# Kernel optimization log

Measured on AMD Instinct MI355X. Metric: run time of the kernel, lower is better.

Reference implementation:

```python
import jax, jax.numpy as jnp
import numpy as np
import math

B, D, TX, TY = 16, 192, 512, 2048
NEG = -1e9


def _neg_cent(x_mean, x_logs, z):
    # x_mean, x_logs: [B, D, TX]; z: [B, D, TY] -> neg_cent: [B, TY, TX]
    s_p_sq_r = jnp.exp(-2.0 * x_logs)                                   # [B,D,TX]
    nc1 = jnp.sum(-0.5 * math.log(2.0 * math.pi) - x_logs, axis=1, keepdims=True)  # [B,1,TX]
    nc2 = jnp.einsum('bdy,bdx->byx', -0.5 * z * z, s_p_sq_r)            # [B,TY,TX]
    nc3 = jnp.einsum('bdy,bdx->byx', z, x_mean * s_p_sq_r)              # [B,TY,TX]
    nc4 = jnp.sum(-0.5 * x_mean * x_mean * s_p_sq_r, axis=1, keepdims=True)  # [B,1,TX]
    return nc1 + nc2 + nc3 + nc4


def _mas_single(nc):
    # Monotonic alignment search (Viterbi DP) for one sample. nc: [TY, TX]
    ty, tx = nc.shape
    xs = jnp.arange(tx)

    def fwd_step(v_prev, inp):
        nc_row, y = inp
        v_diag = jnp.concatenate([jnp.full((1,), NEG, nc.dtype), v_prev[:-1]])
        take_diag = v_diag > v_prev                                      # bool [TX]
        v = nc_row + jnp.maximum(v_prev, v_diag)
        v = jnp.where(xs <= y, v, NEG)                                   # path cannot be ahead of time
        return v, take_diag

    v0 = jnp.where(xs == 0, nc[0], NEG)
    _, dirs = jax.lax.scan(fwd_step, v0, (nc[1:], jnp.arange(1, ty)))    # dirs: [TY-1, TX]

    def bwd_step(idx, d_row):
        # idx = path position at row y; move to y-1
        new_idx = idx - d_row[idx].astype(idx.dtype)
        return new_idx, idx

    idx0, path_tail = jax.lax.scan(bwd_step, jnp.array(tx - 1, jnp.int32), dirs, reverse=True)
    path = jnp.concatenate([idx0[None], path_tail])                      # [TY]
    return jax.nn.one_hot(path, tx, dtype=nc.dtype)                      # [TY, TX]


def _forward(x_mean, x_logs, z, logw):
    neg_cent = jax.lax.stop_gradient(_neg_cent(x_mean, x_logs, z))
    attn = jax.lax.stop_gradient(jax.vmap(_mas_single)(neg_cent))        # [B,TY,TX]
    w = jnp.sum(attn, axis=1, keepdims=True)                             # [B,1,TX] durations
    logw_ = jnp.log(w + 1e-6)
    l_length = jnp.sum((logw - logw_) ** 2, axis=(1, 2))                 # [B]
    m_p = jnp.einsum('byx,bdx->bdy', attn, x_mean)                       # [B,D,TY]
    logs_p = jnp.einsum('byx,bdx->bdy', attn, x_logs)                    # [B,D,TY]
    out_main = jnp.concatenate([m_p, logs_p], axis=1)                    # [B,2D,TY]
    return out_main, l_length, attn


def setup_inputs() -> dict:
    key = jax.random.key(0)
    k1, k2, k3, k4 = jax.random.split(key, 4)
    return {
        'x_mean': jax.random.normal(k1, (B, D, TX), jnp.float32),
        'x_logs': jax.random.normal(k2, (B, D, TX), jnp.float32),
        'z': jax.random.normal(k3, (B, D, TY), jnp.float32),
        'logw': jax.random.normal(k4, (B, 1, TX), jnp.float32),
    }


def reference(x_mean, x_logs, z, logw):
    return _forward(x_mean, x_logs, z, logw)
```

## Files before the change

### kernel.cpp

```cpp
#include <hip/hip_runtime.h>
#include <hip/hip_bf16.h>
#include <math.h>

#define B_   16
#define D_   192
#define TX_  512
#define TY_  2048
#define NEGV (-1e9f)



typedef __attribute__((address_space(1))) const float glob_f;
typedef __attribute__((address_space(3))) float       lds_f;

__global__ __launch_bounds__(512) void precomp(const float* __restrict__ xm,
                                               const float* __restrict__ xl,
                                               float* __restrict__ S,
                                               float* __restrict__ MS,
                                               float* __restrict__ Cpart) {
    int b = blockIdx.x;
    int p = blockIdx.y;
    int x = threadIdx.x;
    size_t base = ((size_t)b * D_ + p * 32) * TX_;
    const float* mb = xm + base;
    const float* lb = xl + base;
    float* Sb  = S  + base;
    float* MSb = MS + base;
    float c = 0.f;
    for (int d = 0; d < 32; d++) {
        float lg = lb[d * TX_ + x];
        float mn = mb[d * TX_ + x];
        float s  = expf(-2.f * lg);
        float ms = mn * s;
        Sb[d * TX_ + x]  = s;
        MSb[d * TX_ + x] = ms;
        c += -0.9189385332046727f - lg - 0.5f * mn * mn * s;
    }
    Cpart[(b * 6 + p) * TX_ + x] = c;
}

__global__ __launch_bounds__(256) void gemm_nc(const float* __restrict__ z,
                                               const float* __restrict__ S,
                                               const float* __restrict__ MS,
                                               const float* __restrict__ Cpart,
                                               float* __restrict__ NC) {
    int bx = blockIdx.x;
    int by = blockIdx.y;
    int b  = blockIdx.z;
    int tid = threadIdx.x;
    int tx = tid & 15, ty = tid >> 4;
    __shared__ __align__(16) float Zt[16 * 128];
    __shared__ __align__(16) float St[16 * 128];
    __shared__ __align__(16) float MSt[16 * 128];

    float acc[8][8];
#pragma unroll
    for (int i = 0; i < 8; i++)
#pragma unroll
        for (int j = 0; j < 8; j++) acc[i][j] = 0.f;

    int x0 = bx * 128, y0 = by * 128;
    const float* zb  = z  + (size_t)b * D_ * TY_;
    const float* Sb  = S  + (size_t)b * D_ * TX_;
    const float* MSb = MS + (size_t)b * D_ * TX_;

    for (int k0 = 0; k0 < D_; k0 += 16) {
#pragma unroll
        for (int j = 0; j < 2; j++) {
            int f = tid + j * 256;
            int kk = f >> 5, c = (f & 31) * 4;
            __builtin_amdgcn_global_load_lds((glob_f*)(zb  + (size_t)(k0 + kk) * TY_ + y0 + c),
                                             (lds_f*)(Zt  + f * 4), 16, 0, 0);
            __builtin_amdgcn_global_load_lds((glob_f*)(Sb  + (size_t)(k0 + kk) * TX_ + x0 + c),
                                             (lds_f*)(St  + f * 4), 16, 0, 0);
            __builtin_amdgcn_global_load_lds((glob_f*)(MSb + (size_t)(k0 + kk) * TX_ + x0 + c),
                                             (lds_f*)(MSt + f * 4), 16, 0, 0);
        }
        __syncthreads();

#pragma unroll 2
        for (int kk = 0; kk < 16; kk++) {
            float4 z0 = *(const float4*)&Zt[kk * 128 + ty * 4];
            float4 z1 = *(const float4*)&Zt[kk * 128 + 64 + ty * 4];
            float4 s0 = *(const float4*)&St[kk * 128 + tx * 4];
            float4 s1 = *(const float4*)&St[kk * 128 + 64 + tx * 4];
            float4 m0 = *(const float4*)&MSt[kk * 128 + tx * 4];
            float4 m1 = *(const float4*)&MSt[kk * 128 + 64 + tx * 4];
            float4 u0, u1;
            u0.x = -0.5f * z0.x * z0.x; u0.y = -0.5f * z0.y * z0.y;
            u0.z = -0.5f * z0.z * z0.z; u0.w = -0.5f * z0.w * z0.w;
            u1.x = -0.5f * z1.x * z1.x; u1.y = -0.5f * z1.y * z1.y;
            u1.z = -0.5f * z1.z * z1.z; u1.w = -0.5f * z1.w * z1.w;
            float zz[8] = {z0.x, z0.y, z0.z, z0.w, z1.x, z1.y, z1.z, z1.w};
            float uu[8] = {u0.x, u0.y, u0.z, u0.w, u1.x, u1.y, u1.z, u1.w};
            float ss[8] = {s0.x, s0.y, s0.z, s0.w, s1.x, s1.y, s1.z, s1.w};
            float mm[8] = {m0.x, m0.y, m0.z, m0.w, m1.x, m1.y, m1.z, m1.w};
#pragma unroll
            for (int i = 0; i < 8; i++)
#pragma unroll
                for (int j = 0; j < 8; j++)
                    acc[i][j] += uu[i] * ss[j] + zz[i] * mm[j];
        }
        __syncthreads();
    }

    float cv[8] = {0, 0, 0, 0, 0, 0, 0, 0};
#pragma unroll
    for (int p = 0; p < 6; p++) {
        float4 c0 = *(const float4*)&Cpart[(b * 6 + p) * TX_ + x0 + tx * 4];
        float4 c1 = *(const float4*)&Cpart[(b * 6 + p) * TX_ + x0 + 64 + tx * 4];
        cv[0] += c0.x; cv[1] += c0.y; cv[2] += c0.z; cv[3] += c0.w;
        cv[4] += c1.x; cv[5] += c1.y; cv[6] += c1.z; cv[7] += c1.w;
    }

#pragma unroll
    for (int i = 0; i < 8; i++) {
        int y = y0 + ty * 4 + (i & 3) + 64 * (i >> 2);
        float4 o0, o1;
        o0.x = acc[i][0] + cv[0]; o0.y = acc[i][1] + cv[1];
        o0.z = acc[i][2] + cv[2]; o0.w = acc[i][3] + cv[3];
        o1.x = acc[i][4] + cv[4]; o1.y = acc[i][5] + cv[5];
        o1.z = acc[i][6] + cv[6]; o1.w = acc[i][7] + cv[7];
        *(float4*)&NC[((size_t)b * TY_ + y) * TX_ + x0 + tx * 4]      = o0;
        *(float4*)&NC[((size_t)b * TY_ + y) * TX_ + x0 + 64 + tx * 4] = o1;
    }
}

__global__ __launch_bounds__(64, 1) void mas_forward(const float* __restrict__ NC,
                                                     unsigned char* __restrict__ dirs) {
    int b = blockIdx.x;
    int lane = threadIdx.x;
    const float* ncb = NC + (size_t)b * TY_ * TX_;
    const float4* base = (const float4*)ncb + lane * 2;

    float4 A[16], C[16];
#pragma unroll
    for (int s = 0; s < 16; s++) {
        A[s] = base[(size_t)(1 + s) * 128];
        C[s] = base[(size_t)(1 + s) * 128 + 1];
    }

    float v[8];
#pragma unroll
    for (int j = 0; j < 8; j++) v[j] = NEGV;
    if (lane == 0) v[0] = ncb[0];

    unsigned char* db = dirs + (size_t)b * 2048 * 64 + lane;

    float bound = NEGV;

    auto row_step = [&](float4 a, float4 c, int y, bool mask) {
        float ncv[8] = {a.x, a.y, a.z, a.w, c.x, c.y, c.z, c.w};
        float vd0 = (lane == 0) ? NEGV : bound;
        float v6o = v[6], v7o = v[7];
        float v7n = ncv[7] + fmaxf(v7o, v6o);
        if (mask && y < 511 && lane * 8 + 7 > y) v7n = NEGV;
        bound = __shfl_up(v7n, 1);
        unsigned bits = (v6o > v7o) ? 0x80u : 0u;
        float vd = vd0;
#pragma unroll
        for (int j = 0; j < 7; j++) {
            float vp = v[j];
            bits |= (vd > vp) ? (1u << j) : 0u;
            v[j] = ncv[j] + fmaxf(vp, vd);
            vd = vp;
        }
        if (mask && y < 511) {
            int xb = lane * 8;
#pragma unroll
            for (int j = 0; j < 7; j++)
                if (xb + j > y) v[j] = NEGV;
        }
        v[7] = v7n;
        db[(size_t)(y - 1) * 64] = (unsigned char)bits;
    };

    int y = 1;
    for (int k = 0; k < 32; k++) {
#pragma unroll
        for (int s = 0; s < 16; s++) {
            float4 a = A[s], c = C[s];
            A[s] = base[(size_t)(y + 16) * 128];
            C[s] = base[(size_t)(y + 16) * 128 + 1];
            row_step(a, c, y, true);
            y++;
        }
    }
    for (int k = 32; k < 127; k++) {
#pragma unroll
        for (int s = 0; s < 16; s++) {
            float4 a = A[s], c = C[s];
            A[s] = base[(size_t)(y + 16) * 128];
            C[s] = base[(size_t)(y + 16) * 128 + 1];
            row_step(a, c, y, false);
            y++;
        }
    }
#pragma unroll
    for (int s = 0; s < 15; s++) {
        row_step(A[s], C[s], y, false);
        y++;
    }
}

__global__ __launch_bounds__(64, 1) void mas_backtrack(const unsigned* __restrict__ dirs,
                                                       int* __restrict__ path) {
    int b = blockIdx.x;
    int lane = threadIdx.x;
    const unsigned* db = dirs + (size_t)b * 2048 * 16;
    int idx = TX_ - 1;

    for (int y_hi = 2047; y_hi >= 1; y_hi -= 64) {
        int wb = (idx >> 5) - 2;
        if (wb < 0) wb = 0;
        int base = wb << 5;
        int y = y_hi - lane;
        unsigned w0 = 0, w1 = 0, w2 = 0;
        if (y >= 1) {
            const unsigned* r = db + (size_t)(y - 1) * 16 + wb;
            w0 = r[0]; w1 = r[1]; w2 = r[2];
        }
        int steps = (y_hi < 64) ? y_hi : 64;
        int my_path = 0;
#pragma unroll 8
        for (int t = 0; t < steps; t++) {
            if (lane == t) my_path = idx;
            unsigned u0 = (unsigned)__shfl((int)w0, t);
            unsigned u1 = (unsigned)__shfl((int)w1, t);
            unsigned u2 = (unsigned)__shfl((int)w2, t);
            int off = idx - base;
            unsigned w = (off < 32) ? u0 : ((off < 64) ? u1 : u2);
            idx -= (int)((w >> (off & 31)) & 1u);
        }
        if (lane < steps) path[b * TY_ + (y_hi - lane)] = my_path;
    }
    if (lane == 0) path[b * TY_ + 0] = idx;
}

__global__ __launch_bounds__(512) void durations_ll(const int* __restrict__ path,
                                                    const float* __restrict__ logw,
                                                    float* __restrict__ out_l) {
    int b = blockIdx.x;
    int tid = threadIdx.x;
    __shared__ int wcnt[TX_];
    __shared__ float partial[8];
    wcnt[tid] = 0;
    __syncthreads();
    for (int y = tid; y < TY_; y += 512)
        atomicAdd(&wcnt[path[b * TY_ + y]], 1);
    __syncthreads();
    float t = logw[b * TX_ + tid] - logf((float)wcnt[tid] + 1e-6f);
    float sq = t * t;
#pragma unroll
    for (int off = 32; off > 0; off >>= 1) sq += __shfl_down(sq, off);
    if ((tid & 63) == 0) partial[tid >> 6] = sq;
    __syncthreads();
    if (tid == 0) {
        float s = 0.f;
#pragma unroll
        for (int i = 0; i < 8; i++) s += partial[i];
        out_l[b] = s;
    }
}

__global__ __launch_bounds__(256) void gather_main(const int* __restrict__ path,
                                                   const float* __restrict__ xm,
                                                   const float* __restrict__ xl,
                                                   float* __restrict__ out) {
    int c = blockIdx.x;
    int b = blockIdx.y;
    int tid = threadIdx.x;
    const float* src = (c < D_) ? (xm + ((size_t)b * D_ + c) * TX_)
                                : (xl + ((size_t)b * D_ + (c - D_)) * TX_);
    const int* pb = path + b * TY_;
    float* ob = out + ((size_t)b * 2 * D_ + c) * TY_;
#pragma unroll
    for (int k = 0; k < 8; k++) {
        int y = tid + k * 256;
        ob[y] = src[pb[y]];
    }
}

__global__ __launch_bounds__(128) void write_attn(const int* __restrict__ path,
                                                  float* __restrict__ attn) {
    int blk = blockIdx.x;
    int b = blk >> 11;
    int y = blk & 2047;
    int tid = threadIdx.x;
    int p = path[b * TY_ + y];
    float4 val = make_float4(0.f, 0.f, 0.f, 0.f);
    if ((p >> 2) == tid) {
        int r = p & 3;
        if (r == 0) val.x = 1.f;
        else if (r == 1) val.y = 1.f;
        else if (r == 2) val.z = 1.f;
        else val.w = 1.f;
    }
    ((float4*)attn)[((size_t)blk) * 128 + tid] = val;
}

extern "C" void kernel_launch(void* const* d_in, const int* in_sizes, int n_in,
                              void* d_out, int out_size, void* d_ws, size_t ws_size,
                              hipStream_t stream) {
    const float* x_mean = (const float*)d_in[0];
    const float* x_logs = (const float*)d_in[1];
    const float* z      = (const float*)d_in[2];
    const float* logw   = (const float*)d_in[3];
    float* out = (float*)d_out;

    char* ws = (char*)d_ws;
    float* S            = (float*)(ws + 0);
    float* MS           = (float*)(ws + 6291456);
    float* NC           = (float*)(ws + 12615680);
    unsigned char* dirs = (unsigned char*)(ws + 79724544);
    float* Cpart        = (float*)(ws + 79724544);
    int* path           = (int*)(ws + 81821696);

    float* out_main = out;
    float* out_l    = out + 12582912;
    float* out_attn = out + 12582928;

    precomp<<<dim3(B_, 6), dim3(512), 0, stream>>>(x_mean, x_logs, S, MS, Cpart);
    gemm_nc<<<dim3(4, 16, 16), dim3(256), 0, stream>>>(z, S, MS, Cpart, NC);
    mas_forward<<<dim3(B_), dim3(64), 0, stream>>>(NC, dirs);
    mas_backtrack<<<dim3(B_), dim3(64), 0, stream>>>((const unsigned*)dirs, path);
    durations_ll<<<dim3(B_), dim3(512), 0, stream>>>(path, logw, out_l);
    gather_main<<<dim3(384, 16), dim3(256), 0, stream>>>(path, x_mean, x_logs, out_main);
    write_attn<<<dim3(B_ * TY_), dim3(128), 0, stream>>>(path, out_attn);
}
```

Baseline: 763.1 us.

## Stage MAS forward rows through an LDS ring via async global-to-LDS loads

Replaces the 16-row register prefetch in the Viterbi forward kernel with a 16-slot LDS ring buffer. Rows are filled 12 rows ahead using global_load_lds, and waits are controlled with explicit s_waitcnt vmcnt counts. Rows are read back from LDS into a three-deep register rotation. The aim is to keep global-memory latency off the serial row chain while cutting register pressure. The cost is an LDS read on every row, and correctness now depends on the hand-tuned vmcnt thresholds, which also count the per-row direction stores.

```diff
diff --git a/kernel.cpp b/kernel.cpp
--- a/kernel.cpp
+++ b/kernel.cpp
@@ -126,19 +126,15 @@
     }
 }
 
+#define RING 16
+#define PF   12
+
 __global__ __launch_bounds__(64, 1) void mas_forward(const float* __restrict__ NC,
                                                      unsigned char* __restrict__ dirs) {
     int b = blockIdx.x;
     int lane = threadIdx.x;
     const float* ncb = NC + (size_t)b * TY_ * TX_;
-    const float4* base = (const float4*)ncb + lane * 2;
-
-    float4 A[16], C[16];
-#pragma unroll
-    for (int s = 0; s < 16; s++) {
-        A[s] = base[(size_t)(1 + s) * 128];
-        C[s] = base[(size_t)(1 + s) * 128 + 1];
-    }
+    __shared__ __align__(16) float ring[RING * TX_];
 
     float v[8];
 #pragma unroll
@@ -146,8 +142,22 @@
     if (lane == 0) v[0] = ncb[0];
 
     unsigned char* db = dirs + (size_t)b * 2048 * 64 + lane;
-
     float bound = NEGV;
+
+    auto stage = [&](int row) {
+        int slot = row & (RING - 1);
+        const float* src = ncb + (size_t)row * TX_ + lane * 4;
+        __builtin_amdgcn_global_load_lds((glob_f*)src,
+                                         (lds_f*)&ring[slot * TX_], 16, 0, 0);
+        __builtin_amdgcn_global_load_lds((glob_f*)(src + 256),
+                                         (lds_f*)&ring[slot * TX_ + 256], 16, 0, 0);
+    };
+
+    auto lds_row = [&](int row, float4& a, float4& c) {
+        int slot = row & (RING - 1);
+        a = *(const float4*)&ring[slot * TX_ + lane * 8];
+        c = *(const float4*)&ring[slot * TX_ + lane * 8 + 4];
+    };
 
     auto row_step = [&](float4 a, float4 c, int y, bool mask) {
         float ncv[8] = {a.x, a.y, a.z, a.w, c.x, c.y, c.z, c.w};
@@ -175,32 +185,48 @@
         db[(size_t)(y - 1) * 64] = (unsigned char)bits;
     };
 
+#pragma unroll
+    for (int r = 1; r <= PF; r++) stage(r);
+    asm volatile("s_waitcnt vmcnt(0)" ::: "memory");
+
+    float4 a0, c0, a1, c1, a2, c2;
+    lds_row(1, a0, c0);
+    lds_row(2, a1, c1);
+
     int y = 1;
-    for (int k = 0; k < 32; k++) {
-#pragma unroll
-        for (int s = 0; s < 16; s++) {
-            float4 a = A[s], c = C[s];
-            A[s] = base[(size_t)(y + 16) * 128];
-            C[s] = base[(size_t)(y + 16) * 128 + 1];
-            row_step(a, c, y, true);
-            y++;
-        }
-    }
-    for (int k = 32; k < 127; k++) {
-#pragma unroll
-        for (int s = 0; s < 16; s++) {
-            float4 a = A[s], c = C[s];
-            A[s] = base[(size_t)(y + 16) * 128];
-            C[s] = base[(size_t)(y + 16) * 128 + 1];
-            row_step(a, c, y, false);
-            y++;
-        }
-    }
-#pragma unroll
-    for (int s = 0; s < 15; s++) {
-        row_step(A[s], C[s], y, false);
-        y++;
-    }
+    for (int t = 0; t < 170; t++) {
+        asm volatile("s_waitcnt vmcnt(28)" ::: "memory");
+        lds_row(y + 2, a2, c2);
+        stage(y + PF);
+        row_step(a0, c0, y, true); y++;
+
+        asm volatile("s_waitcnt vmcnt(28)" ::: "memory");
+        lds_row(y + 2, a0, c0);
+        stage(y + PF);
+        row_step(a1, c1, y, true); y++;
+
+        asm volatile("s_waitcnt vmcnt(28)" ::: "memory");
+        lds_row(y + 2, a1, c1);
+        stage(y + PF);
+        row_step(a2, c2, y, true); y++;
+    }
+    for (int t = 0; t < 512; t++) {
+        asm volatile("s_waitcnt vmcnt(28)" ::: "memory");
+        lds_row(y + 2, a2, c2);
+        stage(min(y + PF, TY_ - 1));
+        row_step(a0, c0, y, false); y++;
+
+        asm volatile("s_waitcnt vmcnt(28)" ::: "memory");
+        lds_row(min(y + 2, TY_ - 1), a0, c0);
+        stage(min(y + PF, TY_ - 1));
+        row_step(a1, c1, y, false); y++;
+
+        asm volatile("s_waitcnt vmcnt(28)" ::: "memory");
+        lds_row(min(y + 2, TY_ - 1), a1, c1);
+        stage(min(y + PF, TY_ - 1));
+        row_step(a2, c2, y, false); y++;
+    }
+    row_step(a0, c0, 2047, false);
 }
 
 __global__ __launch_bounds__(64, 1) void mas_backtrack(const unsigned* __restrict__ dirs,
```

Measured after the change: 1.058 ms. 1.39x slower.

## Hand-pipeline MAS forward loads with inline asm and explicit vmcnt waits

Applied to the files above, without the earlier changes.

Rewrites the serial Viterbi forward kernel to issue global row loads and direction-byte stores through inline asm, keeping a 16-row register ring. Partial s_waitcnt vmcnt(45) waits replace the compiler's conservative full waits, so loads for later rows stay in flight while the current row is computed. It also adds index clamps in backtrack, durations and gather as safety guards. The hand-counted vmcnt is fragile: it relies on the exact count of outstanding loads and stores, and an error would read data before it arrives.

```diff
diff --git a/kernel.cpp b/kernel.cpp
--- a/kernel.cpp
+++ b/kernel.cpp
@@ -12,6 +12,7 @@
 
 typedef __attribute__((address_space(1))) const float glob_f;
 typedef __attribute__((address_space(3))) float       lds_f;
+typedef float f32x4 __attribute__((ext_vector_type(4)));
 
 __global__ __launch_bounds__(512) void precomp(const float* __restrict__ xm,
                                                const float* __restrict__ xl,
@@ -131,25 +132,19 @@
     int b = blockIdx.x;
     int lane = threadIdx.x;
     const float* ncb = NC + (size_t)b * TY_ * TX_;
-    const float4* base = (const float4*)ncb + lane * 2;
-
-    float4 A[16], C[16];
-#pragma unroll
-    for (int s = 0; s < 16; s++) {
-        A[s] = base[(size_t)(1 + s) * 128];
-        C[s] = base[(size_t)(1 + s) * 128 + 1];
-    }
+    int voff = lane * 32;
+
+    float nc00 = ncb[0];
+    asm volatile("" :: "v"(nc00));
 
     float v[8];
 #pragma unroll
     for (int j = 0; j < 8; j++) v[j] = NEGV;
-    if (lane == 0) v[0] = ncb[0];
-
-    unsigned char* db = dirs + (size_t)b * 2048 * 64 + lane;
+    if (lane == 0) v[0] = nc00;
 
     float bound = NEGV;
 
-    auto row_step = [&](float4 a, float4 c, int y, bool mask) {
+    auto row_step = [&](f32x4 a, f32x4 c, int y, bool mask) -> unsigned {
         float ncv[8] = {a.x, a.y, a.z, a.w, c.x, c.y, c.z, c.w};
         float vd0 = (lane == 0) ? NEGV : bound;
         float v6o = v[6], v7o = v[7];
@@ -172,35 +167,113 @@
                 if (xb + j > y) v[j] = NEGV;
         }
         v[7] = v7n;
-        db[(size_t)(y - 1) * 64] = (unsigned char)bits;
+        return bits;
     };
 
+    f32x4 r0a, r0c, r1a, r1c, r2a, r2c, r3a, r3c, r4a, r4c, r5a, r5c, r6a, r6c, r7a, r7c;
+    f32x4 r8a, r8c, r9a, r9c, r10a, r10c, r11a, r11c, r12a, r12c, r13a, r13c, r14a, r14c, r15a, r15c;
+
+    const float* pf = ncb + TX_;
+    unsigned char* dp = dirs + (size_t)b * 2048 * 64;
+
+#define LOADPAIR(RA, RC)                                                   \
+    do {                                                                   \
+        asm volatile("global_load_dwordx4 %0, %2, %1 offset:0"             \
+                     : "=v"(RA) : "s"(pf), "v"(voff));                     \
+        asm volatile("global_load_dwordx4 %0, %2, %1 offset:16"            \
+                     : "=v"(RC) : "s"(pf), "v"(voff));                     \
+        pf += TX_;                                                         \
+    } while (0)
+
+#define STOREBITS(BITS)                                                    \
+    asm volatile("global_store_byte %1, %2, %0" :: "s"(dp), "v"(lane), "v"(BITS))
+
+#define PHASE(RA, RC, MASKED)                                              \
+    do {                                                                   \
+        asm volatile("s_waitcnt vmcnt(45)" : "+v"(RA), "+v"(RC));          \
+        __builtin_amdgcn_sched_barrier(0);                                 \
+        unsigned bits_ = row_step(RA, RC, y, MASKED);                      \
+        STOREBITS(bits_);                                                  \
+        LOADPAIR(RA, RC);                                                  \
+        dp += 64;                                                          \
+        y++;                                                               \
+    } while (0)
+
+#define PH16(MASKED)                                                       \
+    PHASE(r0a, r0c, MASKED);  PHASE(r1a, r1c, MASKED);                     \
+    PHASE(r2a, r2c, MASKED);  PHASE(r3a, r3c, MASKED);                     \
+    PHASE(r4a, r4c, MASKED);  PHASE(r5a, r5c, MASKED);                     \
+    PHASE(r6a, r6c, MASKED);  PHASE(r7a, r7c, MASKED);                     \
+    PHASE(r8a, r8c, MASKED);  PHASE(r9a, r9c, MASKED);                     \
+    PHASE(r10a, r10c, MASKED); PHASE(r11a, r11c, MASKED);                  \
+    PHASE(r12a, r12c, MASKED); PHASE(r13a, r13c, MASKED);                  \
+    PHASE(r14a, r14c, MASKED); PHASE(r15a, r15c, MASKED);
+
+    LOADPAIR(r0a, r0c);   LOADPAIR(r1a, r1c);   LOADPAIR(r2a, r2c);   LOADPAIR(r3a, r3c);
+    LOADPAIR(r4a, r4c);   LOADPAIR(r5a, r5c);   LOADPAIR(r6a, r6c);   LOADPAIR(r7a, r7c);
+    LOADPAIR(r8a, r8c);   LOADPAIR(r9a, r9c);   LOADPAIR(r10a, r10c); LOADPAIR(r11a, r11c);
+    LOADPAIR(r12a, r12c); LOADPAIR(r13a, r13c); LOADPAIR(r14a, r14c); LOADPAIR(r15a, r15c);
+    asm volatile("s_waitcnt vmcnt(0)" ::: "memory");
+    __builtin_amdgcn_sched_barrier(0);
+
     int y = 1;
-    for (int k = 0; k < 32; k++) {
-#pragma unroll
-        for (int s = 0; s < 16; s++) {
-            float4 a = A[s], c = C[s];
-            A[s] = base[(size_t)(y + 16) * 128];
-            C[s] = base[(size_t)(y + 16) * 128 + 1];
-            row_step(a, c, y, true);
-            y++;
-        }
-    }
-    for (int k = 32; k < 127; k++) {
-#pragma unroll
-        for (int s = 0; s < 16; s++) {
-            float4 a = A[s], c = C[s];
-            A[s] = base[(size_t)(y + 16) * 128];
-            C[s] = base[(size_t)(y + 16) * 128 + 1];
-            row_step(a, c, y, false);
-            y++;
-        }
-    }
-#pragma unroll
-    for (int s = 0; s < 15; s++) {
-        row_step(A[s], C[s], y, false);
+    for (int t = 0; t < 32; t++) {
+        PH16(true)
+    }
+    for (int t = 32; t < 126; t++) {
+        PH16(false)
+    }
+    PHASE(r0a, r0c, false);  PHASE(r1a, r1c, false);
+    PHASE(r2a, r2c, false);  PHASE(r3a, r3c, false);
+    PHASE(r4a, r4c, false);  PHASE(r5a, r5c, false);
+    PHASE(r6a, r6c, false);  PHASE(r7a, r7c, false);
+    PHASE(r8a, r8c, false);  PHASE(r9a, r9c, false);
+    PHASE(r10a, r10c, false); PHASE(r11a, r11c, false);
+    PHASE(r12a, r12c, false); PHASE(r13a, r13c, false);
+    PHASE(r14a, r14c, false);
+    {
+        asm volatile("s_waitcnt vmcnt(45)" : "+v"(r15a), "+v"(r15c));
+        __builtin_amdgcn_sched_barrier(0);
+        unsigned bits_ = row_step(r15a, r15c, y, false);
+        STOREBITS(bits_);
+        dp += 64;
         y++;
     }
+
+    asm volatile("s_waitcnt vmcnt(1)"
+                 : "+v"(r0a), "+v"(r0c), "+v"(r1a), "+v"(r1c),
+                   "+v"(r2a), "+v"(r2c), "+v"(r3a), "+v"(r3c),
+                   "+v"(r4a), "+v"(r4c), "+v"(r5a), "+v"(r5c),
+                   "+v"(r6a), "+v"(r6c), "+v"(r7a), "+v"(r7c));
+    asm volatile("s_waitcnt vmcnt(1)"
+                 : "+v"(r8a), "+v"(r8c), "+v"(r9a), "+v"(r9c),
+                   "+v"(r10a), "+v"(r10c), "+v"(r11a), "+v"(r11c),
+                   "+v"(r12a), "+v"(r12c), "+v"(r13a), "+v"(r13c),
+                   "+v"(r14a), "+v"(r14c));
+    __builtin_amdgcn_sched_barrier(0);
+    {
+        unsigned bb;
+        bb = row_step(r0a, r0c, y, false);  STOREBITS(bb); dp += 64; y++;
+        bb = row_step(r1a, r1c, y, false);  STOREBITS(bb); dp += 64; y++;
+        bb = row_step(r2a, r2c, y, false);  STOREBITS(bb); dp += 64; y++;
+        bb = row_step(r3a, r3c, y, false);  STOREBITS(bb); dp += 64; y++;
+        bb = row_step(r4a, r4c, y, false);  STOREBITS(bb); dp += 64; y++;
+        bb = row_step(r5a, r5c, y, false);  STOREBITS(bb); dp += 64; y++;
+        bb = row_step(r6a, r6c, y, false);  STOREBITS(bb); dp += 64; y++;
+        bb = row_step(r7a, r7c, y, false);  STOREBITS(bb); dp += 64; y++;
+        bb = row_step(r8a, r8c, y, false);  STOREBITS(bb); dp += 64; y++;
+        bb = row_step(r9a, r9c, y, false);  STOREBITS(bb); dp += 64; y++;
+        bb = row_step(r10a, r10c, y, false); STOREBITS(bb); dp += 64; y++;
+        bb = row_step(r11a, r11c, y, false); STOREBITS(bb); dp += 64; y++;
+        bb = row_step(r12a, r12c, y, false); STOREBITS(bb); dp += 64; y++;
+        bb = row_step(r13a, r13c, y, false); STOREBITS(bb); dp += 64; y++;
+        bb = row_step(r14a, r14c, y, false); STOREBITS(bb);
+    }
+
+#undef PH16
+#undef PHASE
+#undef STOREBITS
+#undef LOADPAIR
 }
 
 __global__ __launch_bounds__(64, 1) void mas_backtrack(const unsigned* __restrict__ dirs,
@@ -213,6 +286,7 @@
     for (int y_hi = 2047; y_hi >= 1; y_hi -= 64) {
         int wb = (idx >> 5) - 2;
         if (wb < 0) wb = 0;
+        if (wb > 13) wb = 13;
         int base = wb << 5;
         int y = y_hi - lane;
         unsigned w0 = 0, w1 = 0, w2 = 0;
@@ -246,8 +320,11 @@
     __shared__ float partial[8];
     wcnt[tid] = 0;
     __syncthreads();
-    for (int y = tid; y < TY_; y += 512)
-        atomicAdd(&wcnt[path[b * TY_ + y]], 1);
+    for (int y = tid; y < TY_; y += 512) {
+        int p = path[b * TY_ + y];
+        if ((unsigned)p > 511u) p = 0;
+        atomicAdd(&wcnt[p], 1);
+    }
     __syncthreads();
     float t = logw[b * TX_ + tid] - logf((float)wcnt[tid] + 1e-6f);
     float sq = t * t;
@@ -277,7 +354,9 @@
 #pragma unroll
     for (int k = 0; k < 8; k++) {
         int y = tid + k * 256;
-        ob[y] = src[pb[y]];
+        int p = pb[y];
+        if ((unsigned)p > 511u) p = 0;
+        ob[y] = src[p];
     }
 }
 
```

Result: faster. 734.1 us (-3.8%).
